# Performance work log

Measured on AMD Instinct MI355X. Metric: run time of the kernel, lower is better.

Reference implementation:

```python
import jax, jax.numpy as jnp
import numpy as np
import math

B, N = 1, 768
CS, CZ, CH, H, PQ, PV = 384, 128, 16, 12, 4, 8
EPS = 1e-8


def setup_inputs() -> dict:
    key = jax.random.key(0)
    ks = jax.random.split(key, 12)
    def rn(k, shape, scale=1.0):
        return jax.random.normal(k, shape, dtype=jnp.float32) * scale
    s = rn(ks[0], (B, N, CS))
    z = rn(ks[1], (B, N, N, CZ))
    rot, _ = jnp.linalg.qr(rn(ks[2], (B, N, 3, 3)))  # proper-ish rigid rotations
    rot = rot.astype(jnp.float32)
    trans = rn(ks[3], (B, N, 3))
    sc = 0.02
    Wq = rn(ks[4], (CS, H * CH), sc); bq = jnp.zeros((H * CH,), jnp.float32)
    Wkv = rn(ks[5], (CS, 2 * H * CH), sc); bkv = jnp.zeros((2 * H * CH,), jnp.float32)
    Wqp = rn(ks[6], (CS, H * PQ * 3), sc); bqp = jnp.zeros((H * PQ * 3,), jnp.float32)
    Wkvp = rn(ks[7], (CS, H * (PQ + PV) * 3), sc); bkvp = jnp.zeros((H * (PQ + PV) * 3,), jnp.float32)
    Wb = rn(ks[8], (CZ, H), sc); bb = jnp.zeros((H,), jnp.float32)
    head_w = rn(ks[9], (H,), 0.5)
    Wout = rn(ks[10], (H * (CZ + CH + PV * 4), CS), sc); bout = jnp.zeros((CS,), jnp.float32)
    return dict(s=s, z=z, rot=rot, trans=trans, Wq=Wq, bq=bq, Wkv=Wkv, bkv=bkv,
                Wqp=Wqp, bqp=bqp, Wkvp=Wkvp, bkvp=bkvp, Wb=Wb, bb=bb,
                head_w=head_w, Wout=Wout, bout=bout)


def _split_points(x):
    # [B,N,3*M] -> [B,N,M,3]: first M entries are x-coords, next M y, next M z
    return jnp.stack(jnp.split(x, 3, axis=-1), axis=-1)


def _apply_frame(rot, trans, pts):
    # pts [B,N,M,3] -> R @ p + t
    return jnp.einsum('bnxy,bnmy->bnmx', rot, pts) + trans[:, :, None, :]


def reference(s, z, rot, trans, Wq, bq, Wkv, bkv, Wqp, bqp, Wkvp, bkvp, Wb, bb, head_w, Wout, bout):
    # scalar q/k/v: [B,N,H,CH]
    q = (s @ Wq + bq).reshape(B, N, H, CH)
    kv = (s @ Wkv + bkv).reshape(B, N, H, 2 * CH)
    k, v = kv[..., :CH], kv[..., CH:]

    # point q/k/v in global frame
    q_pts = _apply_frame(rot, trans, _split_points(s @ Wqp + bqp)).reshape(B, N, H, PQ, 3)
    kv_pts = _apply_frame(rot, trans, _split_points(s @ Wkvp + bkvp)).reshape(B, N, H, PQ + PV, 3)
    k_pts, v_pts = kv_pts[..., :PQ, :], kv_pts[..., PQ:, :]

    # pair bias [B,N,N,H]
    b = z @ Wb + bb

    # scalar attention logits [B,H,i,j]
    a = jnp.einsum('bihc,bjhc->bhij', q, k) * math.sqrt(1.0 / (3 * CH))
    a = a + math.sqrt(1.0 / 3) * jnp.transpose(b, (0, 3, 1, 2))

    # point-distance attention: [B,i,j,H,PQ]
    diff = q_pts[:, :, None] - k_pts[:, None]          # [B,i,j,H,PQ,3]
    d2 = jnp.sum(diff * diff, axis=-1)                  # [B,i,j,H,PQ]
    hw = jax.nn.softplus(head_w) * math.sqrt(1.0 / (3 * (PQ * 9.0 / 2)))
    pt_att = -0.5 * jnp.sum(d2 * hw[None, None, None, :, None], axis=-1)  # [B,i,j,H]
    a = a + jnp.transpose(pt_att, (0, 3, 1, 2))

    a = jax.nn.softmax(a, axis=-1)                      # [B,H,i,j]

    # scalar output [B,N,H*CH]
    o = jnp.einsum('bhij,bjhc->bihc', a, v).reshape(B, N, H * CH)

    # point output [B,i,H,PV,3], mapped back into local frame of residue i
    o_pt = jnp.einsum('bhij,bjhpx->bihpx', a, v_pts)
    o_pt = jnp.einsum('bnyx,bnhpy->bnhpx', rot, o_pt - trans[:, :, None, None, :])
    o_pt_norm = jnp.sqrt(jnp.sum(o_pt * o_pt, axis=-1) + EPS).reshape(B, N, H * PV)
    o_pt_flat = o_pt.reshape(B, N, H * PV, 3)

    # pair output [B,N,H*CZ]
    o_pair = jnp.einsum('bhij,bijc->bihc', a, z).reshape(B, N, H * CZ)

    cat = jnp.concatenate(
        [o, o_pt_flat[..., 0], o_pt_flat[..., 1], o_pt_flat[..., 2], o_pt_norm, o_pair], axis=-1)
    return cat @ Wout + bout
```

## Files before the change

### kernel.cpp

```cpp
#include <hip/hip_runtime.h>
#include <hip/hip_bf16.h>
#include <cmath>

#define NN 768
#define CS 384
#define CZ 128
#define CH 16
#define HH 12
#define PQ 4
#define PV 8
#define CATC 2112

typedef __attribute__((ext_vector_type(8))) __bf16 bf16x8;
typedef __attribute__((ext_vector_type(8))) unsigned short us8;
typedef __attribute__((ext_vector_type(4))) float f32x4;

__device__ __forceinline__ unsigned short f2bf(float f) {
  unsigned int u = __builtin_bit_cast(unsigned int, f);
  u += 0x7FFFu + ((u >> 16) & 1u);
  return (unsigned short)(u >> 16);
}
__device__ __forceinline__ float bf2f(unsigned short u) {
  return __builtin_bit_cast(float, ((unsigned int)u) << 16);
}
__device__ __forceinline__ unsigned short nf2bf(float f) {
  __bf16 b = (__bf16)f;
  return __builtin_bit_cast(unsigned short, b);
}

__global__ void k_proj(const float* __restrict__ s, const float* __restrict__ rot,
                       const float* __restrict__ trans,
                       const float* __restrict__ Wq, const float* __restrict__ bq,
                       const float* __restrict__ Wkv, const float* __restrict__ bkv,
                       const float* __restrict__ Wqp, const float* __restrict__ bqp,
                       const float* __restrict__ Wkvp, const float* __restrict__ bkvp,
                       float* __restrict__ q, float* __restrict__ kk, float* __restrict__ vv,
                       float* __restrict__ qpts, float* __restrict__ kvpts) {
  __shared__ float srow[CS];
  __shared__ float rawq[144];
  __shared__ float rawkv[432];
  __shared__ float R[9];
  __shared__ float T[3];
  int n = blockIdx.x, t = threadIdx.x;
  for (int u = t; u < CS; u += 256) srow[u] = s[(size_t)n*CS + u];
  if (t < 9) R[t] = rot[(size_t)n*9 + t];
  if (t < 3) T[t] = trans[(size_t)n*3 + t];
  __syncthreads();

  for (int col = t; col < 192; col += 256) {
    float acc = bq[col];
    for (int c = 0; c < CS; c++) acc += srow[c] * Wq[(size_t)c*192 + col];
    q[(size_t)n*192 + col] = acc;
  }
  for (int col = t; col < 384; col += 256) {
    float acc = bkv[col];
    for (int c = 0; c < CS; c++) acc += srow[c] * Wkv[(size_t)c*384 + col];
    int h = col >> 5, u2 = col & 31;
    if (u2 < 16) kk[(size_t)n*192 + h*16 + u2] = acc;
    else         vv[(size_t)n*192 + h*16 + (u2-16)] = acc;
  }
  for (int col = t; col < 144; col += 256) {
    float acc = bqp[col];
    for (int c = 0; c < CS; c++) acc += srow[c] * Wqp[(size_t)c*144 + col];
    rawq[col] = acc;
  }
  for (int col = t; col < 432; col += 256) {
    float acc = bkvp[col];
    for (int c = 0; c < CS; c++) acc += srow[c] * Wkvp[(size_t)c*432 + col];
    rawkv[col] = acc;
  }
  __syncthreads();

  for (int u = t; u < 48*3; u += 256) {
    int m = u / 3, x = u % 3;
    float p0 = rawq[0*48 + m], p1 = rawq[1*48 + m], p2 = rawq[2*48 + m];
    qpts[((size_t)n*48 + m)*3 + x] = R[x*3+0]*p0 + R[x*3+1]*p1 + R[x*3+2]*p2 + T[x];
  }
  for (int u = t; u < 144*3; u += 256) {
    int m = u / 3, x = u % 3;
    float p0 = rawkv[0*144 + m], p1 = rawkv[1*144 + m], p2 = rawkv[2*144 + m];
    kvpts[((size_t)n*144 + m)*3 + x] = R[x*3+0]*p0 + R[x*3+1]*p1 + R[x*3+2]*p2 + T[x];
  }
}

__global__ void k_prep(const float* __restrict__ kk, const float* __restrict__ kvpts,
                       const float* __restrict__ Wb,
                       unsigned short* __restrict__ Bq, unsigned short* __restrict__ afT) {
  int jt16 = blockIdx.x, t = threadIdx.x;
  for (int u = t; u < 768; u += 256) {
    int hp = u >> 6, kg = (u >> 4) & 3, l15 = u & 15;
    int j = jt16*16 + l15;
    unsigned short vals[8];
    #pragma unroll
    for (int e = 0; e < 8; e++) {
      int cc = kg*8 + e;
      float v;
      if (cc < 16) {
        v = kk[(size_t)j*192 + hp*16 + cc];
      } else if (cc < 28) {
        v = kvpts[(size_t)j*432 + hp*36 + (cc-16)];
      } else if (cc == 28) {
        float s2 = 0.f;
        #pragma unroll
        for (int m = 0; m < 12; m++) {
          float d = kvpts[(size_t)j*432 + hp*36 + m];
          s2 += d*d;
        }
        v = s2;
      } else if (cc == 29) {
        v = 1.0f;
      } else {
        v = 0.f;
      }
      vals[e] = f2bf(v);
    }
    *(us8*)(Bq + ((size_t)(jt16*12 + hp)*64 + kg*16 + l15)*8) = *(const us8*)vals;
  }
  if (blockIdx.x == 0) {
    int kg = t >> 6, l15 = (t >> 2) & 15, ks = t & 3;
    unsigned short vals[8];
    #pragma unroll
    for (int kc = 0; kc < 8; kc++) {
      vals[kc] = (l15 < 12)
        ? f2bf(0.5773502691896258f * Wb[(size_t)(ks*32 + kg*8 + kc)*12 + l15])
        : (unsigned short)0;
    }
    *(us8*)(afT + (size_t)t*8) = *(const us8*)vals;
  }
}

__global__ void k_prep_aug(const float* __restrict__ q, const float* __restrict__ qpts,
                           const float* __restrict__ bb, const float* __restrict__ head_w,
                           unsigned short* __restrict__ augT) {
  int g = blockIdx.x*256 + threadIdx.x;
  int i = g >> 6, kg = (g >> 4) & 3, l15 = g & 15;
  const float sc1 = 0.14433756729740643f;
  const float sc3 = 0.5773502691896258f;
  float hw = (l15 < 12) ? log1pf(expf(head_w[l15])) * 0.13608276348795434f : 0.f;
  unsigned short vals[8];
  #pragma unroll
  for (int e = 0; e < 8; e++) {
    int idx = kg*8 + e;
    float v = 0.f;
    if (l15 < 12) {
      if (idx < 16) v = sc1 * q[(size_t)i*192 + l15*16 + idx];
      else if (idx < 28) v = hw * qpts[(size_t)i*144 + l15*12 + (idx-16)];
      else if (idx == 28) v = -0.5f * hw;
      else if (idx == 29) {
        float s2 = 0.f;
        #pragma unroll
        for (int m = 0; m < 12; m++) {
          float d = qpts[(size_t)i*144 + l15*12 + m];
          s2 += d*d;
        }
        v = sc3 * bb[l15] - 0.5f * hw * s2;
      }
    }
    vals[e] = f2bf(v);
  }
  *(us8*)(augT + (size_t)g*8) = *(const us8*)vals;
}

__global__ void k_prep_v(const float* __restrict__ vv, const float* __restrict__ kvpts,
                         unsigned short* __restrict__ Vq) {
  int g = blockIdx.x*256 + threadIdx.x;
  int l15 = g & 15;
  int kg  = (g >> 4) & 3;
  int r2  = g >> 6;
  int ks  = r2 % 24;
  int hn  = r2 / 24;
  int nt  = hn % 3;
  int h   = hn / 3;
  int col = nt*16 + l15;
  unsigned short vals[8];
  #pragma unroll
  for (int e = 0; e < 8; e++) {
    int j = ks*32 + kg*8 + e;
    float v = 0.f;
    if (col < 16)      v = vv[(size_t)j*192 + h*16 + col];
    else if (col < 40) v = kvpts[(size_t)j*432 + h*36 + 12 + (col-16)];
    vals[e] = f2bf(v);
  }
  *(us8*)(Vq + (size_t)g*8) = *(const us8*)vals;
}

#define ZP 72
#define PP 72
__global__ void __launch_bounds__(256) k_zpass(
    const float* __restrict__ z, const unsigned short* __restrict__ Bq,
    const unsigned short* __restrict__ afT, const unsigned short* __restrict__ augT,
    unsigned short* __restrict__ p_bf, float* __restrict__ Pp,
    float* __restrict__ msbuf) {
  __shared__ unsigned short zt[128*ZP];
  __shared__ unsigned short p_l[16*PP];
  __shared__ float redm[4][16];
  __shared__ float reds[4][16];
  int jt = blockIdx.x, i = blockIdx.y, t = threadIdx.x;
  int w = t >> 6, l = t & 63, kg = l >> 4, l15 = l & 15;
  const us8* afT8 = (const us8*)afT;
  const us8* augT8 = (const us8*)augT;
  const us8* Bq8 = (const us8*)Bq;
  us8 zero8 = {0,0,0,0,0,0,0,0};

  us8 af[4];
  #pragma unroll
  for (int ks = 0; ks < 4; ks++) af[ks] = afT8[(kg*16 + l15)*4 + ks];
  us8 aug = augT8[((size_t)i*4 + kg)*16 + l15];

  int jcol = jt*64 + w*16 + l15;
  const float* zr = z + ((size_t)i*NN + jcol)*CZ;
  f32x4 accz = {0.f,0.f,0.f,0.f};
  f32x4 aa0 = {0.f,0.f,0.f,0.f}, aa1 = {0.f,0.f,0.f,0.f}, aa2 = {0.f,0.f,0.f,0.f};
  int js = (w*16 + l15 + kg*16) & 63;
  #pragma unroll
  for (int ks = 0; ks < 4; ks++) {
    float4 z0 = *(const float4*)(zr + ks*32 + kg*8);
    float4 z1 = *(const float4*)(zr + ks*32 + kg*8 + 4);
    bf16x8 bv;
    bv[0] = (__bf16)z0.x; bv[1] = (__bf16)z0.y; bv[2] = (__bf16)z0.z; bv[3] = (__bf16)z0.w;
    bv[4] = (__bf16)z1.x; bv[5] = (__bf16)z1.y; bv[6] = (__bf16)z1.z; bv[7] = (__bf16)z1.w;
    us8 bu = __builtin_bit_cast(us8, bv);
    #pragma unroll
    for (int e = 0; e < 8; e++)
      zt[(ks*32 + kg*8 + e)*ZP + js] = bu[e];
    accz = __builtin_amdgcn_mfma_f32_16x16x32_bf16(
        __builtin_bit_cast(bf16x8, af[ks]), bv, accz, 0, 0, 0);
  }
  int jtile = jt*4 + w;
  #pragma unroll
  for (int hp = 0; hp < 12; hp++) {
    us8 bqv = Bq8[(size_t)(jtile*12 + hp)*64 + kg*16 + l15];
    us8 sel = (l15 == hp) ? aug : zero8;
    f32x4* dst = (hp < 4) ? &aa0 : (hp < 8) ? &aa1 : &aa2;
    *dst = __builtin_amdgcn_mfma_f32_16x16x32_bf16(
        __builtin_bit_cast(bf16x8, sel), __builtin_bit_cast(bf16x8, bqv), *dst, 0, 0, 0);
  }
  f32x4 lg = (accz + aa0) + (aa1 + aa2);

  float mr[4];
  #pragma unroll
  for (int r = 0; r < 4; r++) {
    float m = lg[r];
    #pragma unroll
    for (int off = 1; off < 16; off <<= 1) m = fmaxf(m, __shfl_xor(m, off));
    mr[r] = m;
  }
  if (l15 == 0) {
    #pragma unroll
    for (int r = 0; r < 4; r++) redm[w][kg*4+r] = mr[r];
  }
  __syncthreads();
  float er[4], mloc[4];
  float sr[4];
  #pragma unroll
  for (int r = 0; r < 4; r++) {
    int h = kg*4 + r;
    float m = fmaxf(fmaxf(redm[0][h], redm[1][h]), fmaxf(redm[2][h], redm[3][h]));
    mloc[r] = m;
    float e = expf(lg[r] - m);
    er[r] = e;
    float s = e;
    #pragma unroll
    for (int off = 1; off < 16; off <<= 1) s += __shfl_xor(s, off);
    sr[r] = s;
  }
  if (l15 == 0) {
    #pragma unroll
    for (int r = 0; r < 4; r++) reds[w][kg*4+r] = sr[r];
  }
  __syncthreads();
  #pragma unroll
  for (int r = 0; r < 4; r++) {
    int row = kg*4 + r;
    p_l[row*PP + w*16 + l15] = (kg < 3) ? nf2bf(er[r]) : (unsigned short)0;
  }
  if (w == 0 && l15 == 0 && kg < 3) {
    #pragma unroll
    for (int r = 0; r < 4; r++) {
      int h = kg*4 + r;
      float s_loc = reds[0][h] + reds[1][h] + reds[2][h] + reds[3][h];
      msbuf[((size_t)i*12 + jt)*24 + h]      = mloc[r];
      msbuf[((size_t)i*12 + jt)*24 + 12 + h] = s_loc;
    }
  }
  __syncthreads();

  {
    const us8* pl8 = (const us8*)p_l;
    us8* pg8 = (us8*)(p_bf + (size_t)i*12*768);
    if (t < 96) {
      int h = t >> 3, c8 = t & 7;
      pg8[h*96 + jt*8 + c8] = pl8[h*9 + c8];
    }
  }

  {
    const us8* pl8 = (const us8*)p_l;
    f32x4 acc0 = {0.f,0.f,0.f,0.f}, acc1 = {0.f,0.f,0.f,0.f};
    int c0 = w*32 + l15, c1 = c0 + 16;
    int s0 = (c0 >> 3) & 3, s1 = (c1 >> 3) & 3;
    #pragma unroll
    for (int ks2 = 0; ks2 < 2; ks2++) {
      us8 av = pl8[l15*9 + ks2*4 + kg];
      int j0 = ks2*32 + kg*8;
      us8 b0 = *(const us8*)(zt + (size_t)c0*ZP + ((j0 + s0*16) & 63));
      us8 b1 = *(const us8*)(zt + (size_t)c1*ZP + ((j0 + s1*16) & 63));
      acc0 = __builtin_amdgcn_mfma_f32_16x16x32_bf16(
          __builtin_bit_cast(bf16x8, av), __builtin_bit_cast(bf16x8, b0), acc0, 0, 0, 0);
      acc1 = __builtin_amdgcn_mfma_f32_16x16x32_bf16(
          __builtin_bit_cast(bf16x8, av), __builtin_bit_cast(bf16x8, b1), acc1, 0, 0, 0);
    }
    #pragma unroll
    for (int r = 0; r < 4; r++) {
      int h = kg*4 + r;
      if (h < 12) {
        float* pp = Pp + (((size_t)i*12 + jt)*12 + h)*128;
        pp[c0] = acc0[r];
        pp[c1] = acc1[r];
      }
    }
  }
}

__global__ void k_comb(const float* __restrict__ Pp, const float* __restrict__ msbuf,
                       unsigned short* __restrict__ p_bf, float* __restrict__ cat) {
  __shared__ float alpha[12][12];
  int i = blockIdx.x, t = threadIdx.x;
  if (t < 12) {
    int h = t;
    float ml[12];
    float m = -1e30f;
    #pragma unroll
    for (int jt = 0; jt < 12; jt++) {
      ml[jt] = msbuf[((size_t)i*12 + jt)*24 + h];
      m = fmaxf(m, ml[jt]);
    }
    float s = 0.f;
    float al[12];
    #pragma unroll
    for (int jt = 0; jt < 12; jt++) {
      al[jt] = expf(ml[jt] - m);
      s += msbuf[((size_t)i*12 + jt)*24 + 12 + h] * al[jt];
    }
    float invs = 1.0f / s;
    #pragma unroll
    for (int jt = 0; jt < 12; jt++) alpha[h][jt] = al[jt] * invs;
  }
  __syncthreads();
  for (int u = t; u < 1536; u += 256) {
    int h = u >> 7, c = u & 127;
    float acc = 0.f;
    #pragma unroll
    for (int jt = 0; jt < 12; jt++)
      acc += Pp[(((size_t)i*12 + jt)*12 + h)*128 + c] * alpha[h][jt];
    cat[(size_t)i*CATC + 576 + h*128 + c] = acc;
  }
  us8* pg8 = (us8*)(p_bf + (size_t)i*12*768);
  for (int u = t; u < 1152; u += 256) {
    int h = u / 96, c8 = u % 96, jt = c8 >> 3;
    float a = alpha[h][jt];
    us8 v = pg8[h*96 + c8];
    #pragma unroll
    for (int e = 0; e < 8; e++) v[e] = nf2bf(bf2f(v[e]) * a);
    pg8[h*96 + c8] = v;
  }
}

__global__ void k_ov(const unsigned short* __restrict__ p_bf,
                     const unsigned short* __restrict__ Vq,
                     const float* __restrict__ rot, const float* __restrict__ trans,
                     float* __restrict__ cat) {
  __shared__ float opt[16][28];
  __shared__ float Rl[16][9];
  __shared__ float Tl[16][3];
  int it = blockIdx.x, h = blockIdx.y, t = threadIdx.x;
  int i0 = it*16;
  int w = t >> 6, l = t & 63, kg = l >> 4, l15 = l & 15;
  if (t < 144) Rl[t/9][t%9] = rot[(size_t)(i0 + t/9)*9 + (t%9)];
  if (t >= 192 && t < 240) {
    int u = t - 192;
    Tl[u/3][u%3] = trans[(size_t)(i0 + u/3)*3 + (u%3)];
  }
  f32x4 acc = {0.f,0.f,0.f,0.f};
  if (w < 3) {
    const unsigned short* prow = p_bf + ((size_t)(i0 + l15)*12 + h)*768 + kg*8;
    const us8* vq = (const us8*)Vq + (size_t)(h*3 + w)*24*64 + kg*16 + l15;
    for (int ks = 0; ks < 24; ks++) {
      us8 av = *(const us8*)(prow + ks*32);
      us8 bv = vq[(size_t)ks*64];
      acc = __builtin_amdgcn_mfma_f32_16x16x32_bf16(
          __builtin_bit_cast(bf16x8, av), __builtin_bit_cast(bf16x8, bv), acc, 0, 0, 0);
    }
  }
  if (w == 0) {
    #pragma unroll
    for (int r = 0; r < 4; r++)
      cat[(size_t)(i0 + kg*4 + r)*CATC + h*16 + l15] = acc[r];
  } else if (w == 1) {
    #pragma unroll
    for (int r = 0; r < 4; r++) opt[kg*4 + r][l15] = acc[r];
  } else if (w == 2) {
    if (l15 < 8) {
      #pragma unroll
      for (int r = 0; r < 4; r++) opt[kg*4 + r][16 + l15] = acc[r];
    }
  }
  __syncthreads();
  if (t < 128) {
    int ip = t >> 3, p = t & 7;
    float x0 = opt[ip][p*3+0] - Tl[ip][0];
    float x1 = opt[ip][p*3+1] - Tl[ip][1];
    float x2 = opt[ip][p*3+2] - Tl[ip][2];
    const float* R = Rl[ip];
    float ox = R[0]*x0 + R[3]*x1 + R[6]*x2;
    float oy = R[1]*x0 + R[4]*x1 + R[7]*x2;
    float oz = R[2]*x0 + R[5]*x1 + R[8]*x2;
    float nrm = sqrtf(ox*ox + oy*oy + oz*oz + 1e-8f);
    float* c = cat + (size_t)(i0 + ip)*CATC;
    int m = h*8 + p;
    c[192 + m] = ox; c[288 + m] = oy; c[384 + m] = oz; c[480 + m] = nrm;
  }
}

#define OROWS 3
__global__ void k_out(const float* __restrict__ cat, const float* __restrict__ Wout,
                      const float* __restrict__ bout, float* __restrict__ out) {
  __shared__ float cl[OROWS*CATC];
  int i0 = blockIdx.x*OROWS, t = threadIdx.x;
  for (int idx = t; idx < OROWS*CATC; idx += 384) cl[idx] = cat[(size_t)i0*CATC + idx];
  __syncthreads();
  float acc[OROWS];
  #pragma unroll
  for (int g = 0; g < OROWS; g++) acc[g] = 0.f;
  for (int r = 0; r < CATC; r += 8) {
    float wv[8];
    #pragma unroll
    for (int u = 0; u < 8; u++) wv[u] = Wout[(size_t)(r+u)*384 + t];
    #pragma unroll
    for (int u = 0; u < 8; u++) {
      #pragma unroll
      for (int g = 0; g < OROWS; g++) acc[g] += cl[g*CATC + r + u] * wv[u];
    }
  }
  float bo = bout[t];
  #pragma unroll
  for (int g = 0; g < OROWS; g++) out[(size_t)(i0+g)*384 + t] = acc[g] + bo;
}

extern "C" void kernel_launch(void* const* d_in, const int* in_sizes, int n_in,
                              void* d_out, int out_size, void* d_ws, size_t ws_size,
                              hipStream_t stream) {
  const float* s      = (const float*)d_in[0];
  const float* z      = (const float*)d_in[1];
  const float* rot    = (const float*)d_in[2];
  const float* trans  = (const float*)d_in[3];
  const float* Wq     = (const float*)d_in[4];
  const float* bq     = (const float*)d_in[5];
  const float* Wkv    = (const float*)d_in[6];
  const float* bkv    = (const float*)d_in[7];
  const float* Wqp    = (const float*)d_in[8];
  const float* bqp    = (const float*)d_in[9];
  const float* Wkvp   = (const float*)d_in[10];
  const float* bkvp   = (const float*)d_in[11];
  const float* Wb     = (const float*)d_in[12];
  const float* bb     = (const float*)d_in[13];
  const float* head_w = (const float*)d_in[14];
  const float* Wout   = (const float*)d_in[15];
  const float* bout   = (const float*)d_in[16];
  float* out = (float*)d_out;

  float* ws    = (float*)d_ws;
  float* q     = ws;
  float* kk    = q     + 147456;
  float* vv    = kk    + 147456;
  float* qpts  = vv    + 147456;
  float* kvpts = qpts  + 110592;
  unsigned short* p_bf = (unsigned short*)(kvpts + 331776);
  float* cat   = (float*)(p_bf + 7077888);
  unsigned short* Bq  = (unsigned short*)(cat + 1622016);
  unsigned short* Vq  = Bq + 294912;
  unsigned short* afT = Vq + 884736;
  unsigned short* augT= afT + 2048;
  float* Pp    = (float*)(augT + 393216);
  float* msbuf = Pp + 14155776;

  k_proj<<<768, 256, 0, stream>>>(s, rot, trans, Wq, bq, Wkv, bkv, Wqp, bqp,
                                  Wkvp, bkvp, q, kk, vv, qpts, kvpts);
  k_prep<<<48, 256, 0, stream>>>(kk, kvpts, Wb, Bq, afT);
  k_prep_aug<<<192, 256, 0, stream>>>(q, qpts, bb, head_w, augT);
  k_prep_v<<<432, 256, 0, stream>>>(vv, kvpts, Vq);
  k_zpass<<<dim3(12, 768), 256, 0, stream>>>(z, Bq, afT, augT, p_bf, Pp, msbuf);
  k_comb<<<768, 256, 0, stream>>>(Pp, msbuf, p_bf, cat);
  k_ov<<<dim3(48, 12), 256, 0, stream>>>(p_bf, Vq, rot, trans, cat);
  k_out<<<256, 384, 0, stream>>>(cat, Wout, bout, out);
}
```

Before: 362.4 us.

## Widen z-pass tiles to 128 columns and merge prep kernels into one launch

The z-pass kernel now handles 128 j-columns per block with 512 threads instead of 64 with 256. This halves the number of partial softmax tiles and the size of the partial pair-output buffer that the combine kernel must read and reduce. The z tile in shared memory uses a new XOR-like swizzle with a 128-wide row, and one barrier is removed. The three small prep kernels are fused into a single launch dispatched by block index, which saves launch overhead. In exchange, per-block shared memory is larger, which may lower occupancy.

```diff
diff --git a/kernel.cpp b/kernel.cpp
--- a/kernel.cpp
+++ b/kernel.cpp
@@ -83,118 +83,116 @@
   }
 }
 
-__global__ void k_prep(const float* __restrict__ kk, const float* __restrict__ kvpts,
-                       const float* __restrict__ Wb,
-                       unsigned short* __restrict__ Bq, unsigned short* __restrict__ afT) {
-  int jt16 = blockIdx.x, t = threadIdx.x;
-  for (int u = t; u < 768; u += 256) {
-    int hp = u >> 6, kg = (u >> 4) & 3, l15 = u & 15;
-    int j = jt16*16 + l15;
+__global__ void k_prep_all(const float* __restrict__ kk, const float* __restrict__ kvpts,
+                           const float* __restrict__ Wb, const float* __restrict__ q,
+                           const float* __restrict__ qpts, const float* __restrict__ bb,
+                           const float* __restrict__ head_w, const float* __restrict__ vv,
+                           unsigned short* __restrict__ Bq, unsigned short* __restrict__ afT,
+                           unsigned short* __restrict__ augT, unsigned short* __restrict__ Vq) {
+  int b = blockIdx.x, t = threadIdx.x;
+  if (b < 48) {
+    int jt16 = b;
+    for (int u = t; u < 768; u += 256) {
+      int hp = u >> 6, kg = (u >> 4) & 3, l15 = u & 15;
+      int j = jt16*16 + l15;
+      unsigned short vals[8];
+      #pragma unroll
+      for (int e = 0; e < 8; e++) {
+        int cc = kg*8 + e;
+        float v;
+        if (cc < 16) {
+          v = kk[(size_t)j*192 + hp*16 + cc];
+        } else if (cc < 28) {
+          v = kvpts[(size_t)j*432 + hp*36 + (cc-16)];
+        } else if (cc == 28) {
+          float s2 = 0.f;
+          #pragma unroll
+          for (int m = 0; m < 12; m++) {
+            float d = kvpts[(size_t)j*432 + hp*36 + m];
+            s2 += d*d;
+          }
+          v = s2;
+        } else if (cc == 29) {
+          v = 1.0f;
+        } else {
+          v = 0.f;
+        }
+        vals[e] = f2bf(v);
+      }
+      *(us8*)(Bq + ((size_t)(jt16*12 + hp)*64 + kg*16 + l15)*8) = *(const us8*)vals;
+    }
+    if (b == 0) {
+      int kg = t >> 6, l15 = (t >> 2) & 15, ks = t & 3;
+      unsigned short vals[8];
+      #pragma unroll
+      for (int kc = 0; kc < 8; kc++) {
+        vals[kc] = (l15 < 12)
+          ? f2bf(0.5773502691896258f * Wb[(size_t)(ks*32 + kg*8 + kc)*12 + l15])
+          : (unsigned short)0;
+      }
+      *(us8*)(afT + (size_t)t*8) = *(const us8*)vals;
+    }
+  } else if (b < 240) {
+    int g = (b-48)*256 + t;
+    int i = g >> 6, kg = (g >> 4) & 3, l15 = g & 15;
+    const float sc1 = 0.14433756729740643f;
+    const float sc3 = 0.5773502691896258f;
+    float hw = (l15 < 12) ? log1pf(expf(head_w[l15])) * 0.13608276348795434f : 0.f;
     unsigned short vals[8];
     #pragma unroll
     for (int e = 0; e < 8; e++) {
-      int cc = kg*8 + e;
-      float v;
-      if (cc < 16) {
-        v = kk[(size_t)j*192 + hp*16 + cc];
-      } else if (cc < 28) {
-        v = kvpts[(size_t)j*432 + hp*36 + (cc-16)];
-      } else if (cc == 28) {
-        float s2 = 0.f;
-        #pragma unroll
-        for (int m = 0; m < 12; m++) {
-          float d = kvpts[(size_t)j*432 + hp*36 + m];
-          s2 += d*d;
+      int idx = kg*8 + e;
+      float v = 0.f;
+      if (l15 < 12) {
+        if (idx < 16) v = sc1 * q[(size_t)i*192 + l15*16 + idx];
+        else if (idx < 28) v = hw * qpts[(size_t)i*144 + l15*12 + (idx-16)];
+        else if (idx == 28) v = -0.5f * hw;
+        else if (idx == 29) {
+          float s2 = 0.f;
+          #pragma unroll
+          for (int m = 0; m < 12; m++) {
+            float d = qpts[(size_t)i*144 + l15*12 + m];
+            s2 += d*d;
+          }
+          v = sc3 * bb[l15] - 0.5f * hw * s2;
         }
-        v = s2;
-      } else if (cc == 29) {
-        v = 1.0f;
-      } else {
-        v = 0.f;
       }
       vals[e] = f2bf(v);
     }
-    *(us8*)(Bq + ((size_t)(jt16*12 + hp)*64 + kg*16 + l15)*8) = *(const us8*)vals;
-  }
-  if (blockIdx.x == 0) {
-    int kg = t >> 6, l15 = (t >> 2) & 15, ks = t & 3;
+    *(us8*)(augT + (size_t)g*8) = *(const us8*)vals;
+  } else {
+    int g = (b-240)*256 + t;
+    int l15 = g & 15;
+    int kg  = (g >> 4) & 3;
+    int r2  = g >> 6;
+    int ks  = r2 % 24;
+    int hn  = r2 / 24;
+    int nt  = hn % 3;
+    int h   = hn / 3;
+    int col = nt*16 + l15;
     unsigned short vals[8];
     #pragma unroll
-    for (int kc = 0; kc < 8; kc++) {
-      vals[kc] = (l15 < 12)
-        ? f2bf(0.5773502691896258f * Wb[(size_t)(ks*32 + kg*8 + kc)*12 + l15])
-        : (unsigned short)0;
-    }
-    *(us8*)(afT + (size_t)t*8) = *(const us8*)vals;
-  }
-}
-
-__global__ void k_prep_aug(const float* __restrict__ q, const float* __restrict__ qpts,
-                           const float* __restrict__ bb, const float* __restrict__ head_w,
-                           unsigned short* __restrict__ augT) {
-  int g = blockIdx.x*256 + threadIdx.x;
-  int i = g >> 6, kg = (g >> 4) & 3, l15 = g & 15;
-  const float sc1 = 0.14433756729740643f;
-  const float sc3 = 0.5773502691896258f;
-  float hw = (l15 < 12) ? log1pf(expf(head_w[l15])) * 0.13608276348795434f : 0.f;
-  unsigned short vals[8];
-  #pragma unroll
-  for (int e = 0; e < 8; e++) {
-    int idx = kg*8 + e;
-    float v = 0.f;
-    if (l15 < 12) {
-      if (idx < 16) v = sc1 * q[(size_t)i*192 + l15*16 + idx];
-      else if (idx < 28) v = hw * qpts[(size_t)i*144 + l15*12 + (idx-16)];
-      else if (idx == 28) v = -0.5f * hw;
-      else if (idx == 29) {
-        float s2 = 0.f;
-        #pragma unroll
-        for (int m = 0; m < 12; m++) {
-          float d = qpts[(size_t)i*144 + l15*12 + m];
-          s2 += d*d;
-        }
-        v = sc3 * bb[l15] - 0.5f * hw * s2;
-      }
-    }
-    vals[e] = f2bf(v);
-  }
-  *(us8*)(augT + (size_t)g*8) = *(const us8*)vals;
-}
-
-__global__ void k_prep_v(const float* __restrict__ vv, const float* __restrict__ kvpts,
-                         unsigned short* __restrict__ Vq) {
-  int g = blockIdx.x*256 + threadIdx.x;
-  int l15 = g & 15;
-  int kg  = (g >> 4) & 3;
-  int r2  = g >> 6;
-  int ks  = r2 % 24;
-  int hn  = r2 / 24;
-  int nt  = hn % 3;
-  int h   = hn / 3;
-  int col = nt*16 + l15;
-  unsigned short vals[8];
-  #pragma unroll
-  for (int e = 0; e < 8; e++) {
-    int j = ks*32 + kg*8 + e;
-    float v = 0.f;
-    if (col < 16)      v = vv[(size_t)j*192 + h*16 + col];
-    else if (col < 40) v = kvpts[(size_t)j*432 + h*36 + 12 + (col-16)];
-    vals[e] = f2bf(v);
-  }
-  *(us8*)(Vq + (size_t)g*8) = *(const us8*)vals;
-}
-
-#define ZP 72
-#define PP 72
-__global__ void __launch_bounds__(256) k_zpass(
+    for (int e = 0; e < 8; e++) {
+      int j = ks*32 + kg*8 + e;
+      float v = 0.f;
+      if (col < 16)      v = vv[(size_t)j*192 + h*16 + col];
+      else if (col < 40) v = kvpts[(size_t)j*432 + h*36 + 12 + (col-16)];
+      vals[e] = f2bf(v);
+    }
+    *(us8*)(Vq + (size_t)g*8) = *(const us8*)vals;
+  }
+}
+
+#define PL2 136
+__global__ void __launch_bounds__(512) k_zpass(
     const float* __restrict__ z, const unsigned short* __restrict__ Bq,
     const unsigned short* __restrict__ afT, const unsigned short* __restrict__ augT,
     unsigned short* __restrict__ p_bf, float* __restrict__ Pp,
     float* __restrict__ msbuf) {
-  __shared__ unsigned short zt[128*ZP];
-  __shared__ unsigned short p_l[16*PP];
-  __shared__ float redm[4][16];
-  __shared__ float reds[4][16];
+  __shared__ unsigned short zt[128*128];
+  __shared__ unsigned short p_l[16*PL2];
+  __shared__ float redm[8][16];
+  __shared__ float reds[8][16];
   int jt = blockIdx.x, i = blockIdx.y, t = threadIdx.x;
   int w = t >> 6, l = t & 63, kg = l >> 4, l15 = l & 15;
   const us8* afT8 = (const us8*)afT;
@@ -207,11 +205,11 @@
   for (int ks = 0; ks < 4; ks++) af[ks] = afT8[(kg*16 + l15)*4 + ks];
   us8 aug = augT8[((size_t)i*4 + kg)*16 + l15];
 
-  int jcol = jt*64 + w*16 + l15;
+  int jloc = w*16 + l15;
+  int jcol = jt*128 + jloc;
   const float* zr = z + ((size_t)i*NN + jcol)*CZ;
   f32x4 accz = {0.f,0.f,0.f,0.f};
   f32x4 aa0 = {0.f,0.f,0.f,0.f}, aa1 = {0.f,0.f,0.f,0.f}, aa2 = {0.f,0.f,0.f,0.f};
-  int js = (w*16 + l15 + kg*16) & 63;
   #pragma unroll
   for (int ks = 0; ks < 4; ks++) {
     float4 z0 = *(const float4*)(zr + ks*32 + kg*8);
@@ -221,12 +219,15 @@
     bv[4] = (__bf16)z1.x; bv[5] = (__bf16)z1.y; bv[6] = (__bf16)z1.z; bv[7] = (__bf16)z1.w;
     us8 bu = __builtin_bit_cast(us8, bv);
     #pragma unroll
-    for (int e = 0; e < 8; e++)
-      zt[(ks*32 + kg*8 + e)*ZP + js] = bu[e];
+    for (int e = 0; e < 8; e++) {
+      int c = ks*32 + kg*8 + e;
+      int js = (jloc + 16*((c>>3)&3) + 8*(c&7)) & 127;
+      zt[c*128 + js] = bu[e];
+    }
     accz = __builtin_amdgcn_mfma_f32_16x16x32_bf16(
         __builtin_bit_cast(bf16x8, af[ks]), bv, accz, 0, 0, 0);
   }
-  int jtile = jt*4 + w;
+  int jtile = jt*8 + w;
   #pragma unroll
   for (int hp = 0; hp < 12; hp++) {
     us8 bqv = Bq8[(size_t)(jtile*12 + hp)*64 + kg*16 + l15];
@@ -250,12 +251,13 @@
     for (int r = 0; r < 4; r++) redm[w][kg*4+r] = mr[r];
   }
   __syncthreads();
-  float er[4], mloc[4];
-  float sr[4];
+  float er[4], mloc[4], sr[4];
   #pragma unroll
   for (int r = 0; r < 4; r++) {
     int h = kg*4 + r;
-    float m = fmaxf(fmaxf(redm[0][h], redm[1][h]), fmaxf(redm[2][h], redm[3][h]));
+    float m = redm[0][h];
+    #pragma unroll
+    for (int ww = 1; ww < 8; ww++) m = fmaxf(m, redm[ww][h]);
     mloc[r] = m;
     float e = expf(lg[r] - m);
     er[r] = e;
@@ -268,96 +270,89 @@
     #pragma unroll
     for (int r = 0; r < 4; r++) reds[w][kg*4+r] = sr[r];
   }
-  __syncthreads();
   #pragma unroll
   for (int r = 0; r < 4; r++) {
     int row = kg*4 + r;
-    p_l[row*PP + w*16 + l15] = (kg < 3) ? nf2bf(er[r]) : (unsigned short)0;
-  }
+    p_l[row*PL2 + jloc] = (kg < 3) ? nf2bf(er[r]) : (unsigned short)0;
+  }
+  __syncthreads();
   if (w == 0 && l15 == 0 && kg < 3) {
     #pragma unroll
     for (int r = 0; r < 4; r++) {
       int h = kg*4 + r;
-      float s_loc = reds[0][h] + reds[1][h] + reds[2][h] + reds[3][h];
-      msbuf[((size_t)i*12 + jt)*24 + h]      = mloc[r];
-      msbuf[((size_t)i*12 + jt)*24 + 12 + h] = s_loc;
-    }
-  }
-  __syncthreads();
+      float s_loc = reds[0][h] + reds[1][h] + reds[2][h] + reds[3][h]
+                  + reds[4][h] + reds[5][h] + reds[6][h] + reds[7][h];
+      msbuf[((size_t)i*6 + jt)*24 + h]      = mloc[r];
+      msbuf[((size_t)i*6 + jt)*24 + 12 + h] = s_loc;
+    }
+  }
 
   {
     const us8* pl8 = (const us8*)p_l;
     us8* pg8 = (us8*)(p_bf + (size_t)i*12*768);
-    if (t < 96) {
-      int h = t >> 3, c8 = t & 7;
-      pg8[h*96 + jt*8 + c8] = pl8[h*9 + c8];
+    if (t < 192) {
+      int h = t >> 4, c8 = t & 15;
+      pg8[h*96 + jt*16 + c8] = pl8[h*17 + c8];
     }
   }
 
   {
     const us8* pl8 = (const us8*)p_l;
-    f32x4 acc0 = {0.f,0.f,0.f,0.f}, acc1 = {0.f,0.f,0.f,0.f};
-    int c0 = w*32 + l15, c1 = c0 + 16;
-    int s0 = (c0 >> 3) & 3, s1 = (c1 >> 3) & 3;
-    #pragma unroll
-    for (int ks2 = 0; ks2 < 2; ks2++) {
-      us8 av = pl8[l15*9 + ks2*4 + kg];
-      int j0 = ks2*32 + kg*8;
-      us8 b0 = *(const us8*)(zt + (size_t)c0*ZP + ((j0 + s0*16) & 63));
-      us8 b1 = *(const us8*)(zt + (size_t)c1*ZP + ((j0 + s1*16) & 63));
-      acc0 = __builtin_amdgcn_mfma_f32_16x16x32_bf16(
-          __builtin_bit_cast(bf16x8, av), __builtin_bit_cast(bf16x8, b0), acc0, 0, 0, 0);
-      acc1 = __builtin_amdgcn_mfma_f32_16x16x32_bf16(
-          __builtin_bit_cast(bf16x8, av), __builtin_bit_cast(bf16x8, b1), acc1, 0, 0, 0);
+    f32x4 acc = {0.f,0.f,0.f,0.f};
+    int c = w*16 + l15;
+    int off = 16*((c>>3)&3) + 8*(c&7);
+    #pragma unroll
+    for (int ks = 0; ks < 4; ks++) {
+      us8 av = pl8[l15*17 + ks*4 + kg];
+      us8 b = *(const us8*)(zt + c*128 + ((ks*32 + kg*8 + off) & 127));
+      acc = __builtin_amdgcn_mfma_f32_16x16x32_bf16(
+          __builtin_bit_cast(bf16x8, av), __builtin_bit_cast(bf16x8, b), acc, 0, 0, 0);
     }
     #pragma unroll
     for (int r = 0; r < 4; r++) {
       int h = kg*4 + r;
-      if (h < 12) {
-        float* pp = Pp + (((size_t)i*12 + jt)*12 + h)*128;
-        pp[c0] = acc0[r];
-        pp[c1] = acc1[r];
-      }
+      if (h < 12)
+        Pp[(((size_t)i*6 + jt)*12 + h)*128 + c] = acc[r];
     }
   }
 }
 
 __global__ void k_comb(const float* __restrict__ Pp, const float* __restrict__ msbuf,
                        unsigned short* __restrict__ p_bf, float* __restrict__ cat) {
-  __shared__ float alpha[12][12];
+  __shared__ float alpha[12][6];
   int i = blockIdx.x, t = threadIdx.x;
   if (t < 12) {
     int h = t;
-    float ml[12];
+    float ml[6];
     float m = -1e30f;
     #pragma unroll
-    for (int jt = 0; jt < 12; jt++) {
-      ml[jt] = msbuf[((size_t)i*12 + jt)*24 + h];
+    for (int jt = 0; jt < 6; jt++) {
+      ml[jt] = msbuf[((size_t)i*6 + jt)*24 + h];
       m = fmaxf(m, ml[jt]);
     }
     float s = 0.f;
-    float al[12];
-    #pragma unroll
-    for (int jt = 0; jt < 12; jt++) {
+    float al[6];
+    #pragma unroll
+    for (int jt = 0; jt < 6; jt++) {
       al[jt] = expf(ml[jt] - m);
-      s += msbuf[((size_t)i*12 + jt)*24 + 12 + h] * al[jt];
+      s += msbuf[((size_t)i*6 + jt)*24 + 12 + h] * al[jt];
     }
     float invs = 1.0f / s;
     #pragma unroll
-    for (int jt = 0; jt < 12; jt++) alpha[h][jt] = al[jt] * invs;
+    for (int jt = 0; jt < 6; jt++) alpha[h][jt] = al[jt] * invs;
   }
   __syncthreads();
   for (int u = t; u < 1536; u += 256) {
     int h = u >> 7, c = u & 127;
     float acc = 0.f;
     #pragma unroll
-    for (int jt = 0; jt < 12; jt++)
-      acc += Pp[(((size_t)i*12 + jt)*12 + h)*128 + c] * alpha[h][jt];
+    for (int jt = 0; jt < 6; jt++)
+      acc += Pp[(((size_t)i*6 + jt)*12 + h)*128 + c] * alpha[h][jt];
     cat[(size_t)i*CATC + 576 + h*128 + c] = acc;
   }
   us8* pg8 = (us8*)(p_bf + (size_t)i*12*768);
   for (int u = t; u < 1152; u += 256) {
-    int h = u / 96, c8 = u % 96, jt = c8 >> 3;
+    int h = u / 96, c8 = u % 96, jt = c8 >> 4;
     float a = alpha[h][jt];
     us8 v = pg8[h*96 + c8];
     #pragma unroll
@@ -482,14 +477,13 @@
   unsigned short* afT = Vq + 884736;
   unsigned short* augT= afT + 2048;
   float* Pp    = (float*)(augT + 393216);
-  float* msbuf = Pp + 14155776;
+  float* msbuf = Pp + 7077888;
 
   k_proj<<<768, 256, 0, stream>>>(s, rot, trans, Wq, bq, Wkv, bkv, Wqp, bqp,
                                   Wkvp, bkvp, q, kk, vv, qpts, kvpts);
-  k_prep<<<48, 256, 0, stream>>>(kk, kvpts, Wb, Bq, afT);
-  k_prep_aug<<<192, 256, 0, stream>>>(q, qpts, bb, head_w, augT);
-  k_prep_v<<<432, 256, 0, stream>>>(vv, kvpts, Vq);
-  k_zpass<<<dim3(12, 768), 256, 0, stream>>>(z, Bq, afT, augT, p_bf, Pp, msbuf);
+  k_prep_all<<<672, 256, 0, stream>>>(kk, kvpts, Wb, q, qpts, bb, head_w, vv,
+                                      Bq, afT, augT, Vq);
+  k_zpass<<<dim3(6, 768), 512, 0, stream>>>(z, Bq, afT, augT, p_bf, Pp, msbuf);
   k_comb<<<768, 256, 0, stream>>>(Pp, msbuf, p_bf, cat);
   k_ov<<<dim3(48, 12), 256, 0, stream>>>(p_bf, Vq, rot, trans, cat);
   k_out<<<256, 384, 0, stream>>>(cat, Wout, bout, out);
```

Result: faster. 301.5 us (-16.8%).
